# Kernel optimization log

Measured on AMD Instinct MI355X. Metric: run time of the kernel, lower is better.

## Reference

```python
import jax, jax.numpy as jnp
import numpy as np

B, H, W, C = 32, 32, 32, 768
E = 4          # num_experts
TOPK = 2
HD = int(C * 0.25)  # 192, expert hidden dim


def setup_inputs() -> dict:
    key = jax.random.key(0)
    ks = jax.random.split(key, 7)
    x = jax.random.normal(ks[0], (B, H, W, C), dtype=jnp.float32)
    # router: nn.Linear(C, E), weight [E, C] init N(0, 0.02), bias zeros
    router_w = jax.random.normal(ks[1], (E, C), dtype=jnp.float32) * 0.02
    router_b = jnp.zeros((E,), dtype=jnp.float32)
    # per-expert MLP: fc1 [E, HD, C], fc2 [E, C, HD] (torch Linear weight layout)
    fc1_w = jax.random.normal(ks[2], (E, HD, C), dtype=jnp.float32) * (1.0 / np.sqrt(C))
    fc1_b = jax.random.normal(ks[3], (E, HD), dtype=jnp.float32) * 0.01
    fc2_w = jax.random.normal(ks[4], (E, C, HD), dtype=jnp.float32) * (1.0 / np.sqrt(HD))
    fc2_b = jax.random.normal(ks[5], (E, C), dtype=jnp.float32) * 0.01
    return {"x": x, "router_w": router_w, "router_b": router_b,
            "fc1_w": fc1_w, "fc1_b": fc1_b, "fc2_w": fc2_w, "fc2_b": fc2_b}


def reference(x, router_w, router_b, fc1_w, fc1_b, fc2_w, fc2_b):
    b, h, w, c = x.shape
    xt = x.reshape(b, h * w, c)                              # [B, S, C]
    # --- router: softmax + top-k + renormalize ---
    logits = jnp.einsum('bsc,ec->bse', xt, router_w) + router_b
    probs = jax.nn.softmax(logits, axis=-1)                  # [B, S, E]
    topk_w, topk_idx = jax.lax.top_k(probs, TOPK)            # [B, S, K]
    topk_w = topk_w / (jnp.sum(topk_w, axis=-1, keepdims=True) + 1e-8)
    # per-expert combine weight: sum over k of weight where idx==e -> [B, S, E]
    combine = jnp.sum(jax.nn.one_hot(topk_idx, E, dtype=xt.dtype)
                      * topk_w[..., None], axis=-2)          # [B, S, E]
    # --- all experts densely (same math as masked gather/scatter) ---
    # fc1 + exact GELU: [B, S, E, HD]
    hmid = jax.nn.gelu(jnp.einsum('bsc,ehc->bseh', xt, fc1_w) + fc1_b,
                       approximate=False)
    # weight tokens before fc2 to avoid [B,S,E,C] intermediate
    hw = hmid * combine[..., None]                           # [B, S, E, HD]
    out = jnp.einsum('bseh,ech->bsc', hw, fc2_w)
    out = out + jnp.einsum('bse,ec->bsc', combine, fc2_b)    # weighted fc2 bias
    return out.reshape(b, h, w, c)
```

## Files before the change

kernel.cpp:

```cpp
#include <hip/hip_runtime.h>
#include <hip/hip_bf16.h>
#include <math.h>

typedef __attribute__((ext_vector_type(8))) __bf16 bf16x8;
typedef __attribute__((ext_vector_type(4))) float f32x4;
typedef __attribute__((ext_vector_type(4))) unsigned short u16x4;

#define TOKENS 32768
#define CDIM   768
#define SLOTCAP 33536
#define MT_TILES 262
#define RBLOCKS 1024

__device__ __forceinline__ void async_copy16(const void* g, void* l) {
    __builtin_amdgcn_global_load_lds(
        (const __attribute__((address_space(1))) void*)g,
        (__attribute__((address_space(3))) void*)l, 16, 0, 0);
}

__device__ __forceinline__ float fast_gelu(float v) {
    float x  = v * 0.70710678118654752f;
    float ax = fabsf(x);
    float t  = __builtin_amdgcn_rcpf(1.0f + 0.3275911f * ax);
    float poly = t * (0.254829592f +
                 t * (-0.284496736f +
                 t * (1.421413741f +
                 t * (-1.453152027f +
                 t * 1.061405429f))));
    float erfv = 1.0f - poly * __expf(-x * x);
    erfv = copysignf(erfv, x);
    return 0.5f * v * (1.0f + erfv);
}

__device__ __forceinline__ int pair_lo(int p) { return p < 3 ? 0 : (p < 5 ? 1 : 2); }
__device__ __forceinline__ int pair_hi(int p) { return p < 3 ? p + 1 : (p < 5 ? p - 1 : 3); }

__device__ __forceinline__ void bucket_offs(const int* __restrict__ meta, int* offs) {
    int run = 0;
#pragma unroll
    for (int p = 0; p < 6; ++p) {
        offs[p] = run;
        run += ((meta[p] + 127) >> 7) << 7;
    }
}

__global__ __launch_bounds__(256) void prep_weights(
    const float* __restrict__ fc1w, const float* __restrict__ fc2w,
    __hip_bfloat16* __restrict__ b1, __hip_bfloat16* __restrict__ b2t,
    int* __restrict__ slots, float2* __restrict__ swt, int* __restrict__ meta)
{
    int idx = blockIdx.x * 256 + threadIdx.x;
    if (idx < 32) meta[idx] = 0;
    if (idx < SLOTCAP) { slots[idx] = -1; swt[idx] = make_float2(0.f, 0.f); }
    b1[idx] = __float2bfloat16(fc1w[idx]);
    int c = idx / 768;
    int r = idx - c * 768;
    int e = r / 192;
    int h = r - e * 192;
    b2t[idx] = __float2bfloat16(fc2w[((size_t)e * 768 + c) * 192 + h]);
}

__global__ __launch_bounds__(256) void router_convert(
    const float* __restrict__ x, const float* __restrict__ rw,
    const float* __restrict__ rb,
    __hip_bfloat16* __restrict__ xb,
    int* __restrict__ pairid, float2* __restrict__ wpair, int* __restrict__ meta)
{
    __shared__ int rc[6];
    if (threadIdx.x < 6) rc[threadIdx.x] = 0;
    __syncthreads();

    const int wave = threadIdx.x >> 6;
    const int lane = threadIdx.x & 63;
    const int wid  = blockIdx.x * 4 + wave;
    const int el   = lane * 4;

    float4 wv[4][3];
#pragma unroll
    for (int e = 0; e < 4; ++e)
#pragma unroll
        for (int t = 0; t < 3; ++t)
            wv[e][t] = *(const float4*)(rw + e * CDIM + t * 256 + el);
    float rbv[4];
#pragma unroll
    for (int e = 0; e < 4; ++e) rbv[e] = rb[e];

    for (int it = 0; it < 8; ++it) {
        const int token = wid * 8 + it;
        const float* xr = x + (size_t)token * CDIM;

        float4 v[3];
#pragma unroll
        for (int t = 0; t < 3; ++t) v[t] = *(const float4*)(xr + t * 256 + el);

        unsigned short* xrow = (unsigned short*)xb + (size_t)token * CDIM;
#pragma unroll
        for (int t = 0; t < 3; ++t) {
            alignas(8) __hip_bfloat16 hb[4];
            hb[0] = __float2bfloat16(v[t].x);
            hb[1] = __float2bfloat16(v[t].y);
            hb[2] = __float2bfloat16(v[t].z);
            hb[3] = __float2bfloat16(v[t].w);
            *(u16x4*)(xrow + t * 256 + el) = *(const u16x4*)hb;
        }

        float s[4];
#pragma unroll
        for (int e = 0; e < 4; ++e) {
            s[e] = v[0].x * wv[e][0].x + v[0].y * wv[e][0].y
                 + v[0].z * wv[e][0].z + v[0].w * wv[e][0].w
                 + v[1].x * wv[e][1].x + v[1].y * wv[e][1].y
                 + v[1].z * wv[e][1].z + v[1].w * wv[e][1].w
                 + v[2].x * wv[e][2].x + v[2].y * wv[e][2].y
                 + v[2].z * wv[e][2].z + v[2].w * wv[e][2].w;
        }
#pragma unroll
        for (int e = 0; e < 4; ++e) {
            float vv = s[e];
            vv += __shfl_xor(vv, 32); vv += __shfl_xor(vv, 16); vv += __shfl_xor(vv, 8);
            vv += __shfl_xor(vv, 4);  vv += __shfl_xor(vv, 2);  vv += __shfl_xor(vv, 1);
            s[e] = vv;
        }
        float lg[4], p[4];
#pragma unroll
        for (int e = 0; e < 4; ++e) lg[e] = s[e] + rbv[e];
        float mx = fmaxf(fmaxf(lg[0], lg[1]), fmaxf(lg[2], lg[3]));
        float ps = 0.f;
#pragma unroll
        for (int e = 0; e < 4; ++e) { p[e] = __expf(lg[e] - mx); ps += p[e]; }
#pragma unroll
        for (int e = 0; e < 4; ++e) p[e] /= ps;
        int a = 0;
#pragma unroll
        for (int e = 1; e < 4; ++e) if (p[e] > p[a]) a = e;
        int b = (a == 0) ? 1 : 0;
#pragma unroll
        for (int e = 0; e < 4; ++e) if (e != a && p[e] > p[b]) b = e;
        float wsum = p[a] + p[b] + 1e-8f;
        if (lane == 0) {
            int lo = a < b ? a : b;
            int hi = a < b ? b : a;
            int pid = (lo == 0) ? hi - 1 : (lo == 1 ? hi + 1 : 5);
            pairid[token] = pid;
            wpair[token] = make_float2(p[lo] / wsum, p[hi] / wsum);
            atomicAdd(&rc[pid], 1);
        }
    }
    __syncthreads();
    if (threadIdx.x < 6 && rc[threadIdx.x])
        atomicAdd(&meta[threadIdx.x], rc[threadIdx.x]);
}

__global__ __launch_bounds__(256) void scatter_tokens(
    const int* __restrict__ pairid, const float2* __restrict__ wpair,
    int* __restrict__ slots, float2* __restrict__ swt, int* __restrict__ meta)
{
    __shared__ int sc[6], sb[6], soff[6];
    int tid = threadIdx.x;
    if (tid < 6) sc[tid] = 0;
    __syncthreads();
    int t = blockIdx.x * 256 + tid;
    int p = pairid[t];
    int r = atomicAdd(&sc[p], 1);
    __syncthreads();
    if (tid == 0) {
        int offs[6];
        bucket_offs(meta, offs);
#pragma unroll
        for (int q = 0; q < 6; ++q) soff[q] = offs[q];
    }
    if (tid < 6) sb[tid] = sc[tid] ? atomicAdd(&meta[16 + tid], sc[tid]) : 0;
    __syncthreads();
    int pos = soff[p] + sb[p] + r;
    slots[pos] = t;
    swt[pos] = wpair[t];
}

__global__ __launch_bounds__(512) void fc1_moe(
    const __hip_bfloat16* __restrict__ A,
    const __hip_bfloat16* __restrict__ Bt,
    const int* __restrict__ slots, const float2* __restrict__ swt,
    const int* __restrict__ meta, const float* __restrict__ bias1,
    __hip_bfloat16* __restrict__ HW)
{
    extern __shared__ __hip_bfloat16 dynsm[];
    __hip_bfloat16* Asm = dynsm;
    __hip_bfloat16* Bsm = dynsm + 2 * 128 * 64;

    const int tid = threadIdx.x;
    const int wave = tid >> 6, lane = tid & 63;
    const int wm = (wave >> 2) * 64;
    const int wn = (wave & 3) * 96;
    const int lrow = lane & 15, quad = lane >> 4;

    constexpr int nwg = MT_TILES;
    constexpr int q = nwg >> 3, rr = nwg & 7;
    const int bid = blockIdx.x;
    const int xcd = bid & 7, sidx = bid >> 3;
    const int by = (xcd < rr ? xcd * (q + 1) : rr * (q + 1) + (xcd - rr) * q) + sidx;
    const int rowA0 = by * 128;

    int offs[6];
    bucket_offs(meta, offs);
    int pb = 0;
#pragma unroll
    for (int i = 1; i < 6; ++i) pb += (rowA0 >= offs[i]) ? 1 : 0;
    const int lo = pair_lo(pb), hi = pair_hi(pb);

    const int srow = lane >> 3;
    const int scol = ((lane & 7) ^ srow) * 8;

    unsigned aoff[2];
    __hip_bfloat16* ldsA[2];
#pragma unroll
    for (int p = 0; p < 2; ++p) {
        int c = wave * 2 + p;
        int tok = slots[rowA0 + c * 8 + srow];
        tok = tok < 0 ? 0 : tok;
        aoff[p] = (unsigned)tok * 768u + scol;
        ldsA[p] = Asm + c * 8 * 64;
    }
    unsigned boff[6];
    __hip_bfloat16* ldsB[6];
#pragma unroll
    for (int p = 0; p < 6; ++p) {
        int c = wave * 6 + p;
        int grow = c * 8 + srow;
        int gb = (grow < 192) ? lo * 192 + grow : hi * 192 + (grow - 192);
        boff[p] = (unsigned)gb * 768u + scol;
        ldsB[p] = Bsm + c * 8 * 64;
    }

    auto stage = [&](int buf, int k0) {
#pragma unroll
        for (int p = 0; p < 2; ++p)
            async_copy16(A + aoff[p] + k0, ldsA[p] + buf * (128 * 64));
#pragma unroll
        for (int p = 0; p < 6; ++p)
            async_copy16(Bt + boff[p] + k0, ldsB[p] + buf * (384 * 64));
    };

    f32x4 acc[4][6] = {};

    stage(0, 0);
    __syncthreads();
#pragma unroll
    for (int it = 0; it < 12; ++it) {
        if (it + 1 < 12) stage((it + 1) & 1, (it + 1) * 64);
        const __hip_bfloat16* As = Asm + (it & 1) * (128 * 64);
        const __hip_bfloat16* Bs = Bsm + (it & 1) * (384 * 64);
#pragma unroll
        for (int kk = 0; kk < 64; kk += 32) {
            bf16x8 af[4], bfr[6];
#pragma unroll
            for (int i = 0; i < 4; ++i) {
                int row = wm + i * 16 + lrow;
                int gp = ((kk >> 3) + quad) ^ (lrow & 7);
                af[i] = *(const bf16x8*)(&As[row * 64 + gp * 8]);
            }
#pragma unroll
            for (int j = 0; j < 6; ++j) {
                int row = wn + j * 16 + lrow;
                int gp = ((kk >> 3) + quad) ^ (lrow & 7);
                bfr[j] = *(const bf16x8*)(&Bs[row * 64 + gp * 8]);
            }
#pragma unroll
            for (int i = 0; i < 4; ++i)
#pragma unroll
                for (int j = 0; j < 6; ++j)
                    acc[i][j] = __builtin_amdgcn_mfma_f32_16x16x32_bf16(
                        af[i], bfr[j], acc[i][j], 0, 0, 0);
        }
        __syncthreads();
    }

    float b1v[6];
#pragma unroll
    for (int j = 0; j < 6; ++j) {
        int col = wn + j * 16 + lrow;
        int ng = (col < 192) ? lo * 192 + col : hi * 192 + (col - 192);
        b1v[j] = bias1[ng];
    }
#pragma unroll
    for (int i = 0; i < 4; ++i) {
#pragma unroll
        for (int r = 0; r < 4; ++r) {
            int rowl = wm + i * 16 + quad * 4 + r;
            float2 wv = swt[rowA0 + rowl];
            __hip_bfloat16* sr = dynsm + rowl * 384 + wn + lrow;
#pragma unroll
            for (int j = 0; j < 6; ++j) {
                float cwt = ((wn + j * 16) >= 192) ? wv.y : wv.x;
                float v = fast_gelu(acc[i][j][r] + b1v[j]) * cwt;
                sr[j * 16] = __float2bfloat16(v);
            }
        }
    }
    __syncthreads();
#pragma unroll
    for (int t = 0; t < 12; ++t) {
        int idx = t * 512 + tid;
        int row = idx / 48;
        int c = idx - row * 48;
        *(uint4*)(HW + (size_t)(rowA0 + row) * 384 + c * 8) =
            *(const uint4*)(dynsm + row * 384 + c * 8);
    }
}

#define BM 128
#define BN 128
#define BK 64

__global__ __launch_bounds__(256) void fc2_moe(
    const __hip_bfloat16* __restrict__ A,
    const __hip_bfloat16* __restrict__ Bt,
    const int* __restrict__ slots, const float2* __restrict__ swt,
    const int* __restrict__ meta, const float* __restrict__ bias2,
    float* __restrict__ OUT)
{
    __shared__ __hip_bfloat16 smem[BM * BK * 4];

    const int tid = threadIdx.x;
    const int wave = tid >> 6, lane = tid & 63;
    const int wm = (wave >> 1) * 64, wn = (wave & 1) * 64;
    const int lrow = lane & 15, quad = lane >> 4;

    constexpr int NT = 6;
    constexpr int nwg = MT_TILES * NT;
    constexpr int q = nwg >> 3, rr = nwg & 7;
    const int bid = blockIdx.x;
    const int xcd = bid & 7, sidx = bid >> 3;
    const int wg = (xcd < rr ? xcd * (q + 1) : rr * (q + 1) + (xcd - rr) * q) + sidx;
    const int by = wg / NT;
    const int bx = wg - by * NT;
    const int rowB0 = bx * BN;
    const int rowA0 = by * BM;

    int offs[6];
    bucket_offs(meta, offs);
    int pb = 0;
#pragma unroll
    for (int i = 1; i < 6; ++i) pb += (rowA0 >= offs[i]) ? 1 : 0;
    const int lo = pair_lo(pb), hi = pair_hi(pb);

    const int srow = lane >> 3;
    const int scol = ((lane & 7) ^ srow) * 8;

    size_t aoff[4], boff[4];
    __hip_bfloat16* ldsA[4];
#pragma unroll
    for (int p = 0; p < 4; ++p) {
        int c = wave * 4 + p;
        int arow = c * 8 + srow;
        aoff[p] = (size_t)(rowA0 + arow) * 384 + scol;
        boff[p] = (size_t)(rowB0 + arow) * 768 + scol;
        ldsA[p] = smem + c * 8 * BK;
    }

    auto stage = [&](int buf, int k0) {
        int bo = buf * (2 * BM * BK);
        size_t badd = (size_t)(k0 < 192 ? lo * 192 : hi * 192 - 192) + k0;
#pragma unroll
        for (int p = 0; p < 4; ++p) {
            async_copy16(A + aoff[p] + k0, ldsA[p] + bo);
            async_copy16(Bt + boff[p] + badd, ldsA[p] + bo + BM * BK);
        }
    };

    f32x4 acc[4][4] = {};
    constexpr int NIT = 384 / BK;

    stage(0, 0);
    __syncthreads();
#pragma unroll
    for (int it = 0; it < NIT; ++it) {
        if (it + 1 < NIT) stage((it + 1) & 1, (it + 1) * BK);
        const __hip_bfloat16* As = smem + (it & 1) * (2 * BM * BK);
        const __hip_bfloat16* Bs = As + BM * BK;
#pragma unroll
        for (int kk = 0; kk < BK; kk += 32) {
            bf16x8 af[4], bfr[4];
#pragma unroll
            for (int i = 0; i < 4; ++i) {
                int row = wm + i * 16 + lrow;
                int gp = ((kk >> 3) + quad) ^ (lrow & 7);
                af[i] = *(const bf16x8*)(&As[row * BK + gp * 8]);
            }
#pragma unroll
            for (int j = 0; j < 4; ++j) {
                int row = wn + j * 16 + lrow;
                int gp = ((kk >> 3) + quad) ^ (lrow & 7);
                bfr[j] = *(const bf16x8*)(&Bs[row * BK + gp * 8]);
            }
#pragma unroll
            for (int i = 0; i < 4; ++i)
#pragma unroll
                for (int j = 0; j < 4; ++j)
                    acc[i][j] = __builtin_amdgcn_mfma_f32_16x16x32_bf16(
                        af[i], bfr[j], acc[i][j], 0, 0, 0);
        }
        __syncthreads();
    }

    float blo[4], bhi[4];
#pragma unroll
    for (int j = 0; j < 4; ++j) {
        int col = rowB0 + wn + j * 16 + lrow;
        blo[j] = bias2[lo * 768 + col];
        bhi[j] = bias2[hi * 768 + col];
    }
    float* smf = (float*)smem;
#pragma unroll
    for (int i = 0; i < 4; ++i) {
#pragma unroll
        for (int r = 0; r < 4; ++r) {
            int rowl = wm + i * 16 + quad * 4 + r;
            float2 wv = swt[rowA0 + rowl];
            float* sr = smf + rowl * BN + wn + lrow;
#pragma unroll
            for (int j = 0; j < 4; ++j)
                sr[j * 16] = acc[i][j][r] + wv.x * blo[j] + wv.y * bhi[j];
        }
    }
    __syncthreads();
#pragma unroll
    for (int t = 0; t < 16; ++t) {
        int idx = t * 256 + tid;
        int row = idx >> 5;
        int ch  = idx & 31;
        int tok = slots[rowA0 + row];
        if (tok >= 0)
            *(float4*)(OUT + (size_t)tok * CDIM + rowB0 + ch * 4) =
                *(const float4*)(smf + row * BN + ch * 4);
    }
}

extern "C" void kernel_launch(void* const* d_in, const int* in_sizes, int n_in,
                              void* d_out, int out_size, void* d_ws, size_t ws_size,
                              hipStream_t stream)
{
    const float* x    = (const float*)d_in[0];
    const float* rw   = (const float*)d_in[1];
    const float* rb   = (const float*)d_in[2];
    const float* fc1w = (const float*)d_in[3];
    const float* fc1b = (const float*)d_in[4];
    const float* fc2w = (const float*)d_in[5];
    const float* fc2b = (const float*)d_in[6];
    float* out = (float*)d_out;

    char* ws = (char*)d_ws;
    __hip_bfloat16* xb   = (__hip_bfloat16*)(ws);
    __hip_bfloat16* hw   = (__hip_bfloat16*)(ws + 50331648);
    __hip_bfloat16* b1   = (__hip_bfloat16*)(ws + 76087296);
    __hip_bfloat16* b2t  = (__hip_bfloat16*)(ws + 77266944);
    float2*         wpr  = (float2*)       (ws + 78446592);
    float2*         swt  = (float2*)       (ws + 78708736);
    int*            pid  = (int*)          (ws + 78977024);
    int*            slots= (int*)          (ws + 79108096);
    int*            meta = (int*)          (ws + 79242240);

    prep_weights<<<2304, 256, 0, stream>>>(fc1w, fc2w, b1, b2t, slots, swt, meta);
    router_convert<<<RBLOCKS, 256, 0, stream>>>(x, rw, rb, xb, pid, wpr, meta);
    scatter_tokens<<<TOKENS / 256, 256, 0, stream>>>(pid, wpr, slots, swt, meta);

    fc1_moe<<<MT_TILES, 512, 131072, stream>>>(
        xb, b1, slots, swt, meta, fc1b, hw);
    fc2_moe<<<MT_TILES * 6, 256, 0, stream>>>(
        hw, b2t, slots, swt, meta, fc2b, out);
}
```

Measured before the change: 288.9 us.

## Pre-gather routed token rows and retile fc1 into 128x128 blocks

Adds a separate gather kernel that copies each slot's token row from the bf16 input into a contiguous buffer, with zero rows for padding slots. The fc1 GEMM then reads A with plain contiguous addressing. fc1 is also retiled from one 128x384 tile per 512-thread block with 128KB of dynamic LDS to three 128x128 tiles per 256-thread block with static LDS, which gives more blocks and likely higher occupancy. The cost is an extra kernel launch plus about 50MB of extra global traffic for the gathered copy, and each A tile is now loaded three times instead of once.

Result: no change. 294.1 us (+1.8%).

```diff
diff --git a/kernel.cpp b/kernel.cpp
--- a/kernel.cpp
+++ b/kernel.cpp
@@ -176,29 +176,48 @@
     swt[pos] = wpair[t];
 }
 
-__global__ __launch_bounds__(512) void fc1_moe(
+__global__ __launch_bounds__(256) void gather_rows(
+    const __hip_bfloat16* __restrict__ xb, const int* __restrict__ slots,
+    __hip_bfloat16* __restrict__ xg)
+{
+    int idx = blockIdx.x * 256 + threadIdx.x;
+    int slot = idx / 96;
+    int ch = idx - slot * 96;
+    int tok = slots[slot];
+    uint4 v = make_uint4(0u, 0u, 0u, 0u);
+    if (tok >= 0)
+        v = *(const uint4*)(xb + (size_t)tok * CDIM + ch * 8);
+    *(uint4*)(xg + (size_t)slot * CDIM + ch * 8) = v;
+}
+
+#define BM 128
+#define BN 128
+#define BK 64
+
+__global__ __launch_bounds__(256) void fc1_moe(
     const __hip_bfloat16* __restrict__ A,
     const __hip_bfloat16* __restrict__ Bt,
-    const int* __restrict__ slots, const float2* __restrict__ swt,
+    const float2* __restrict__ swt,
     const int* __restrict__ meta, const float* __restrict__ bias1,
     __hip_bfloat16* __restrict__ HW)
 {
-    extern __shared__ __hip_bfloat16 dynsm[];
-    __hip_bfloat16* Asm = dynsm;
-    __hip_bfloat16* Bsm = dynsm + 2 * 128 * 64;
+    __shared__ __hip_bfloat16 smem[BM * BK * 4];
 
     const int tid = threadIdx.x;
     const int wave = tid >> 6, lane = tid & 63;
-    const int wm = (wave >> 2) * 64;
-    const int wn = (wave & 3) * 96;
+    const int wm = (wave >> 1) * 64, wn = (wave & 1) * 64;
     const int lrow = lane & 15, quad = lane >> 4;
 
-    constexpr int nwg = MT_TILES;
+    constexpr int NT = 3;
+    constexpr int nwg = MT_TILES * NT;
     constexpr int q = nwg >> 3, rr = nwg & 7;
     const int bid = blockIdx.x;
     const int xcd = bid & 7, sidx = bid >> 3;
-    const int by = (xcd < rr ? xcd * (q + 1) : rr * (q + 1) + (xcd - rr) * q) + sidx;
-    const int rowA0 = by * 128;
+    const int wg = (xcd < rr ? xcd * (q + 1) : rr * (q + 1) + (xcd - rr) * q) + sidx;
+    const int by = wg / NT;
+    const int bx = wg - by * NT;
+    const int rowB0 = bx * BN;
+    const int rowA0 = by * BM;
 
     int offs[6];
     bucket_offs(meta, offs);
@@ -210,74 +229,68 @@
     const int srow = lane >> 3;
     const int scol = ((lane & 7) ^ srow) * 8;
 
-    unsigned aoff[2];
-    __hip_bfloat16* ldsA[2];
-#pragma unroll
-    for (int p = 0; p < 2; ++p) {
-        int c = wave * 2 + p;
-        int tok = slots[rowA0 + c * 8 + srow];
-        tok = tok < 0 ? 0 : tok;
-        aoff[p] = (unsigned)tok * 768u + scol;
-        ldsA[p] = Asm + c * 8 * 64;
-    }
-    unsigned boff[6];
-    __hip_bfloat16* ldsB[6];
-#pragma unroll
-    for (int p = 0; p < 6; ++p) {
-        int c = wave * 6 + p;
-        int grow = c * 8 + srow;
+    size_t aoff[4], boff[4];
+    __hip_bfloat16* ldsA[4];
+#pragma unroll
+    for (int p = 0; p < 4; ++p) {
+        int c = wave * 4 + p;
+        int arow = c * 8 + srow;
+        aoff[p] = (size_t)(rowA0 + arow) * 768 + scol;
+        int grow = rowB0 + arow;
         int gb = (grow < 192) ? lo * 192 + grow : hi * 192 + (grow - 192);
-        boff[p] = (unsigned)gb * 768u + scol;
-        ldsB[p] = Bsm + c * 8 * 64;
+        boff[p] = (size_t)gb * 768 + scol;
+        ldsA[p] = smem + c * 8 * BK;
     }
 
     auto stage = [&](int buf, int k0) {
-#pragma unroll
-        for (int p = 0; p < 2; ++p)
-            async_copy16(A + aoff[p] + k0, ldsA[p] + buf * (128 * 64));
-#pragma unroll
-        for (int p = 0; p < 6; ++p)
-            async_copy16(Bt + boff[p] + k0, ldsB[p] + buf * (384 * 64));
+        int bo = buf * (2 * BM * BK);
+#pragma unroll
+        for (int p = 0; p < 4; ++p) {
+            async_copy16(A + aoff[p] + k0, ldsA[p] + bo);
+            async_copy16(Bt + boff[p] + k0, ldsA[p] + bo + BM * BK);
+        }
     };
 
-    f32x4 acc[4][6] = {};
+    f32x4 acc[4][4] = {};
+    constexpr int NIT = 768 / BK;
 
     stage(0, 0);
     __syncthreads();
 #pragma unroll
-    for (int it = 0; it < 12; ++it) {
-        if (it + 1 < 12) stage((it + 1) & 1, (it + 1) * 64);
-        const __hip_bfloat16* As = Asm + (it & 1) * (128 * 64);
-        const __hip_bfloat16* Bs = Bsm + (it & 1) * (384 * 64);
-#pragma unroll
-        for (int kk = 0; kk < 64; kk += 32) {
-            bf16x8 af[4], bfr[6];
+    for (int it = 0; it < NIT; ++it) {
+        if (it + 1 < NIT) stage((it + 1) & 1, (it + 1) * BK);
+        const __hip_bfloat16* As = smem + (it & 1) * (2 * BM * BK);
+        const __hip_bfloat16* Bs = As + BM * BK;
+#pragma unroll
+        for (int kk = 0; kk < BK; kk += 32) {
+            bf16x8 af[4], bfr[4];
 #pragma unroll
             for (int i = 0; i < 4; ++i) {
                 int row = wm + i * 16 + lrow;
                 int gp = ((kk >> 3) + quad) ^ (lrow & 7);
-                af[i] = *(const bf16x8*)(&As[row * 64 + gp * 8]);
+                af[i] = *(const bf16x8*)(&As[row * BK + gp * 8]);
             }
 #pragma unroll
-            for (int j = 0; j < 6; ++j) {
+            for (int j = 0; j < 4; ++j) {
                 int row = wn + j * 16 + lrow;
                 int gp = ((kk >> 3) + quad) ^ (lrow & 7);
-                bfr[j] = *(const bf16x8*)(&Bs[row * 64 + gp * 8]);
+                bfr[j] = *(const bf16x8*)(&Bs[row * BK + gp * 8]);
             }
 #pragma unroll
             for (int i = 0; i < 4; ++i)
 #pragma unroll
-                for (int j = 0; j < 6; ++j)
+                for (int j = 0; j < 4; ++j)
                     acc[i][j] = __builtin_amdgcn_mfma_f32_16x16x32_bf16(
                         af[i], bfr[j], acc[i][j], 0, 0, 0);
         }
         __syncthreads();
     }
 
-    float b1v[6];
-#pragma unroll
-    for (int j = 0; j < 6; ++j) {
-        int col = wn + j * 16 + lrow;
+    const bool hf = (rowB0 + wn) >= 192;
+    float b1v[4];
+#pragma unroll
+    for (int j = 0; j < 4; ++j) {
+        int col = rowB0 + wn + j * 16 + lrow;
         int ng = (col < 192) ? lo * 192 + col : hi * 192 + (col - 192);
         b1v[j] = bias1[ng];
     }
@@ -287,29 +300,25 @@
         for (int r = 0; r < 4; ++r) {
             int rowl = wm + i * 16 + quad * 4 + r;
             float2 wv = swt[rowA0 + rowl];
-            __hip_bfloat16* sr = dynsm + rowl * 384 + wn + lrow;
-#pragma unroll
-            for (int j = 0; j < 6; ++j) {
-                float cwt = ((wn + j * 16) >= 192) ? wv.y : wv.x;
+            float cwt = hf ? wv.y : wv.x;
+            __hip_bfloat16* srow_p = &smem[rowl * BN + wn + lrow];
+#pragma unroll
+            for (int j = 0; j < 4; ++j) {
                 float v = fast_gelu(acc[i][j][r] + b1v[j]) * cwt;
-                sr[j * 16] = __float2bfloat16(v);
+                srow_p[j * 16] = __float2bfloat16(v);
             }
         }
     }
     __syncthreads();
 #pragma unroll
-    for (int t = 0; t < 12; ++t) {
-        int idx = t * 512 + tid;
-        int row = idx / 48;
-        int c = idx - row * 48;
-        *(uint4*)(HW + (size_t)(rowA0 + row) * 384 + c * 8) =
-            *(const uint4*)(dynsm + row * 384 + c * 8);
-    }
-}
-
-#define BM 128
-#define BN 128
-#define BK 64
+    for (int t = 0; t < 8; ++t) {
+        int idx = t * 256 + tid;
+        int row = idx >> 4;
+        int c16 = (idx & 15) * 8;
+        *(uint4*)(HW + (size_t)(rowA0 + row) * 384 + rowB0 + c16) =
+            *(const uint4*)(&smem[row * BN + c16]);
+    }
+}
 
 __global__ __launch_bounds__(256) void fc2_moe(
     const __hip_bfloat16* __restrict__ A,
@@ -450,21 +459,23 @@
 
     char* ws = (char*)d_ws;
     __hip_bfloat16* xb   = (__hip_bfloat16*)(ws);
-    __hip_bfloat16* hw   = (__hip_bfloat16*)(ws + 50331648);
-    __hip_bfloat16* b1   = (__hip_bfloat16*)(ws + 76087296);
-    __hip_bfloat16* b2t  = (__hip_bfloat16*)(ws + 77266944);
-    float2*         wpr  = (float2*)       (ws + 78446592);
-    float2*         swt  = (float2*)       (ws + 78708736);
-    int*            pid  = (int*)          (ws + 78977024);
-    int*            slots= (int*)          (ws + 79108096);
-    int*            meta = (int*)          (ws + 79242240);
+    __hip_bfloat16* xg   = (__hip_bfloat16*)(ws + 50331648);
+    __hip_bfloat16* hw   = (__hip_bfloat16*)(ws + 101842944);
+    __hip_bfloat16* b1   = (__hip_bfloat16*)(ws + 127598592);
+    __hip_bfloat16* b2t  = (__hip_bfloat16*)(ws + 128778240);
+    float2*         wpr  = (float2*)       (ws + 129957888);
+    float2*         swt  = (float2*)       (ws + 130220032);
+    int*            pid  = (int*)          (ws + 130488320);
+    int*            slots= (int*)          (ws + 130619392);
+    int*            meta = (int*)          (ws + 130753536);
 
     prep_weights<<<2304, 256, 0, stream>>>(fc1w, fc2w, b1, b2t, slots, swt, meta);
     router_convert<<<RBLOCKS, 256, 0, stream>>>(x, rw, rb, xb, pid, wpr, meta);
     scatter_tokens<<<TOKENS / 256, 256, 0, stream>>>(pid, wpr, slots, swt, meta);
-
-    fc1_moe<<<MT_TILES, 512, 131072, stream>>>(
-        xb, b1, slots, swt, meta, fc1b, hw);
+    gather_rows<<<SLOTCAP * 96 / 256, 256, 0, stream>>>(xb, slots, xg);
+
+    fc1_moe<<<MT_TILES * 3, 256, 0, stream>>>(
+        xg, b1, swt, meta, fc1b, hw);
     fc2_moe<<<MT_TILES * 6, 256, 0, stream>>>(
         hw, b2t, slots, swt, meta, fc2b, out);
 }
```
